# Kernel optimization log

Measured on AMD Instinct MI355X. Metric: run time of the kernel, lower is better.

The kernel has to match this reference:

```python
import jax, jax.numpy as jnp
import numpy as np

N_NODES = 20000
N_EDGES = 320000
T = 12
IN_DIM = 128
HID = 256
OUT = 128
HEADS = 4
NEG_SLOPE = 0.2


def _glorot(key, shape, fan_in):
    return jax.random.normal(key, shape, jnp.float32) * (1.0 / np.sqrt(fan_in))


def setup_inputs() -> dict:
    key = jax.random.key(0)
    ks = jax.random.split(key, 12)
    x = jax.random.normal(ks[0], (N_NODES, T, IN_DIM), jnp.float32)
    edge_index = jax.random.randint(ks[1], (2, N_EDGES), 0, N_NODES, jnp.int64)
    return {
        "x": x,
        "edge_index": edge_index,
        "W1": _glorot(ks[2], (IN_DIM, HID), IN_DIM),
        "a_src1": _glorot(ks[3], (HEADS, HID // HEADS), HID // HEADS),
        "a_dst1": _glorot(ks[4], (HEADS, HID // HEADS), HID // HEADS),
        "b1": jnp.zeros((HID,), jnp.float32),
        "W2": _glorot(ks[5], (HID, HID), HID),
        "a_src2": _glorot(ks[6], (HEADS, HID // HEADS), HID // HEADS),
        "a_dst2": _glorot(ks[7], (HEADS, HID // HEADS), HID // HEADS),
        "b2": jnp.zeros((HID,), jnp.float32),
        "W3": _glorot(ks[8], (HID, OUT), HID),
        "a_src3": _glorot(ks[9], (HEADS, OUT // HEADS), OUT // HEADS),
        "a_dst3": _glorot(ks[10], (HEADS, OUT // HEADS), OUT // HEADS),
        "b3": jnp.zeros((OUT,), jnp.float32),
    }


def gat_conv(x, src, dst, W, a_src, a_dst, bias):
    # GATConv (v1), concat=True, add_self_loops=False, negative_slope=0.2
    n = x.shape[0]
    H, C = a_src.shape
    h = (x @ W).reshape(n, H, C)                       # [N,H,C]
    alpha_s = jnp.sum(h * a_src[None], axis=-1)        # [N,H]
    alpha_d = jnp.sum(h * a_dst[None], axis=-1)        # [N,H]
    e = jax.nn.leaky_relu(alpha_s[src] + alpha_d[dst], NEG_SLOPE)  # [E,H]
    e_max = jax.ops.segment_max(e, dst, num_segments=n)           # [N,H]
    e_max = jnp.where(jnp.isfinite(e_max), e_max, 0.0)
    w = jnp.exp(e - e_max[dst])                        # [E,H]
    denom = jax.ops.segment_sum(w, dst, num_segments=n)           # [N,H]
    alpha = w / (denom[dst] + 1e-16)                   # [E,H]
    msg = h[src] * alpha[:, :, None]                   # [E,H,C]
    out = jax.ops.segment_sum(msg, dst, num_segments=n)           # [N,H,C]
    return out.reshape(n, H * C) + bias


def reference(x, edge_index, W1, a_src1, a_dst1, b1, W2, a_src2, a_dst2, b2,
              W3, a_src3, a_dst3, b3):
    src, dst = edge_index[0], edge_index[1]

    def net(xt):  # xt: [N, F]
        h = jax.nn.relu(gat_conv(xt, src, dst, W1, a_src1, a_dst1, b1))
        h = jax.nn.relu(gat_conv(h, src, dst, W2, a_src2, a_dst2, b2))
        return gat_conv(h, src, dst, W3, a_src3, a_dst3, b3)

    xt = jnp.transpose(x, (1, 0, 2))                   # [T,N,F]
    _, out = jax.lax.scan(lambda c, xi: (c, net(xi)), None, xt)
    return jnp.transpose(out, (1, 0, 2))               # [N,T,OUT]
```

## Files before the change

### kernel.cpp

```cpp
#include <hip/hip_runtime.h>
#include <cstdint>
#include <cstddef>
#include <type_traits>

#define N_NODES 20000
#define N_EDGES 320000
#define T_STEPS 12
#define HEADS   4
#define NEG_SLOPE 0.2f

typedef unsigned short u16;
typedef unsigned int   u32;

using bf16x8 = __attribute__((ext_vector_type(8))) __bf16;
using f32x4v = __attribute__((ext_vector_type(4))) float;


__global__ void hist_kernel(const int* __restrict__ dst, int* __restrict__ cnt) {
    int e = blockIdx.x * 256 + threadIdx.x;
    if (e < N_EDGES) atomicAdd(&cnt[dst[e]], 1);
}

__global__ __launch_bounds__(1024) void scan_kernel(const int* __restrict__ cnt,
                                                    int* __restrict__ rp) {
    __shared__ int sd[1024];
    __shared__ int sbase;
    int tid = threadIdx.x;
    if (tid == 0) sbase = 0;
    __syncthreads();
    for (int chunk = 0; chunk < N_NODES; chunk += 1024) {
        int i = chunk + tid;
        int v = (i < N_NODES) ? cnt[i] : 0;
        sd[tid] = v;
        __syncthreads();
        #pragma unroll
        for (int off = 1; off < 1024; off <<= 1) {
            int t = (tid >= off) ? sd[tid - off] : 0;
            __syncthreads();
            sd[tid] += t;
            __syncthreads();
        }
        int incl = sd[tid];
        int base = sbase;
        if (i < N_NODES) rp[i] = base + incl - v;
        __syncthreads();
        if (tid == 1023) sbase = base + incl;
        __syncthreads();
    }
    if (tid == 0) rp[N_NODES] = sbase;
}

__global__ void scatter_kernel(const int* __restrict__ src, const int* __restrict__ dst,
                               const int* __restrict__ rp, int* __restrict__ tmp,
                               int* __restrict__ col) {
    int e = blockIdx.x * 256 + threadIdx.x;
    if (e < N_EDGES) {
        int d = dst[e];
        int pos = rp[d] + atomicAdd(&tmp[d], 1);
        col[pos] = src[e];
    }
}


#define SPLIT2(fx, fy, H, L) do {                                          \
    u32 u0_ = __float_as_uint(fx), u1_ = __float_as_uint(fy);              \
    u32 r0_ = u0_ + 0x7fffu + ((u0_ >> 16) & 1u);                          \
    u32 r1_ = u1_ + 0x7fffu + ((u1_ >> 16) & 1u);                          \
    (H) = (r1_ & 0xffff0000u) | (r0_ >> 16);                               \
    float e0_ = (fx) - __uint_as_float(r0_ & 0xffff0000u);                 \
    float e1_ = (fy) - __uint_as_float(r1_ & 0xffff0000u);                 \
    u32 v0_ = __float_as_uint(e0_), v1_ = __float_as_uint(e1_);            \
    v0_ += 0x7fffu + ((v0_ >> 16) & 1u);                                   \
    v1_ += 0x7fffu + ((v1_ >> 16) & 1u);                                   \
    (L) = (v1_ & 0xffff0000u) | (v0_ >> 16);                               \
} while (0)

__global__ void wsplit_kernel(const float* __restrict__ W, u16* __restrict__ Wh,
                              u16* __restrict__ Wl, int K, int N) {
    int idx = blockIdx.x * 256 + threadIdx.x;
    if (idx >= K * N) return;
    int k = idx / N, n = idx - k * N;
    float f = W[idx];
    u32 u = __float_as_uint(f);
    u32 r = u + 0x7fffu + ((u >> 16) & 1u);
    u16 hb = (u16)(r >> 16);
    float lf = f - __uint_as_float(r & 0xffff0000u);
    u32 v = __float_as_uint(lf);
    v = v + 0x7fffu + ((v >> 16) & 1u);
    Wh[(size_t)n * K + k] = hb;
    Wl[(size_t)n * K + k] = (u16)(v >> 16);
}


template <typename AT>
__global__ __launch_bounds__(256) void gemm_mfma(
        const AT* __restrict__ A, const u16* __restrict__ Bh,
        const u16* __restrict__ Bl, _Float16* __restrict__ Y,
        int Mrows, int Ncols, int K, int strideT, int tbase, int nT) {
    constexpr bool A_F32 = std::is_same<AT, float>::value;
    __shared__ u16 As_h[128][40];
    __shared__ u16 As_l[128][40];
    __shared__ u16 Bs_h[128][40];
    __shared__ u16 Bs_l[128][40];

    int tid  = threadIdx.x;
    int wave = tid >> 6, lane = tid & 63;
    int wr = wave >> 1, wc = wave & 1;
    int fr = lane & 15, fg = lane >> 4;
    int row0 = blockIdx.x * 128;
    int col0 = blockIdx.y * 128;

    int am = tid >> 1;
    int ak = (tid & 1) << 4;
    const AT* ap = nullptr;
    {
        int r = row0 + am;
        if (r < Mrows) {
            int n = r / nT, tl = r - n * nT;
            ap = A + ((size_t)n * strideT + (size_t)(tbase + tl)) * (size_t)K + ak;
        }
    }
    int bn = tid >> 1;
    int bk = (tid & 1) << 4;
    const u16* bph = Bh + (size_t)(col0 + bn) * K + bk;
    const u16* bpl = Bl + (size_t)(col0 + bn) * K + bk;

    f32x4v acc[4][4] = {};

    float4 fa4[4];
    uint4  ra[2];
    uint4 vbh0, vbh1, vbl0, vbl1;

#define LOAD_TILE(K0) do {                                                  \
    if (ap) {                                                               \
        if (A_F32) {                                                        \
            const float* p_ = (const float*)ap + (K0);                      \
            fa4[0] = *(const float4*)(p_);      fa4[1] = *(const float4*)(p_ + 4);  \
            fa4[2] = *(const float4*)(p_ + 8);  fa4[3] = *(const float4*)(p_ + 12); \
        } else {                                                            \
            const _Float16* p_ = (const _Float16*)ap + (K0);                \
            ra[0] = *(const uint4*)(p_);  ra[1] = *(const uint4*)(p_ + 8);  \
        }                                                                   \
    } else {                                                                \
        fa4[0] = fa4[1] = fa4[2] = fa4[3] = make_float4(0.f, 0.f, 0.f, 0.f);\
        ra[0] = ra[1] = make_uint4(0, 0, 0, 0);                             \
    }                                                                       \
    vbh0 = *(const uint4*)(bph + (K0));  vbh1 = *(const uint4*)(bph + (K0) + 8); \
    vbl0 = *(const uint4*)(bpl + (K0));  vbl1 = *(const uint4*)(bpl + (K0) + 8); \
} while (0)

    LOAD_TILE(0);

    for (int k0 = 0; k0 < K; k0 += 32) {
        float fv[16];
        if (A_F32) {
            fv[0]=fa4[0].x; fv[1]=fa4[0].y; fv[2]=fa4[0].z; fv[3]=fa4[0].w;
            fv[4]=fa4[1].x; fv[5]=fa4[1].y; fv[6]=fa4[1].z; fv[7]=fa4[1].w;
            fv[8]=fa4[2].x; fv[9]=fa4[2].y; fv[10]=fa4[2].z; fv[11]=fa4[2].w;
            fv[12]=fa4[3].x; fv[13]=fa4[3].y; fv[14]=fa4[3].z; fv[15]=fa4[3].w;
        } else {
            const _Float16* hx = (const _Float16*)ra;
            #pragma unroll
            for (int i = 0; i < 16; ++i) fv[i] = (float)hx[i];
        }
        u32 h0, h1, h2, h3, h4, h5, h6, h7;
        u32 l0, l1, l2, l3, l4, l5, l6, l7;
        SPLIT2(fv[0],  fv[1],  h0, l0); SPLIT2(fv[2],  fv[3],  h1, l1);
        SPLIT2(fv[4],  fv[5],  h2, l2); SPLIT2(fv[6],  fv[7],  h3, l3);
        SPLIT2(fv[8],  fv[9],  h4, l4); SPLIT2(fv[10], fv[11], h5, l5);
        SPLIT2(fv[12], fv[13], h6, l6); SPLIT2(fv[14], fv[15], h7, l7);
        *(uint4*)&As_h[am][ak]     = make_uint4(h0, h1, h2, h3);
        *(uint4*)&As_h[am][ak + 8] = make_uint4(h4, h5, h6, h7);
        *(uint4*)&As_l[am][ak]     = make_uint4(l0, l1, l2, l3);
        *(uint4*)&As_l[am][ak + 8] = make_uint4(l4, l5, l6, l7);
        *(uint4*)&Bs_h[bn][bk]     = vbh0;
        *(uint4*)&Bs_h[bn][bk + 8] = vbh1;
        *(uint4*)&Bs_l[bn][bk]     = vbl0;
        *(uint4*)&Bs_l[bn][bk + 8] = vbl1;
        __syncthreads();

        if (k0 + 32 < K) LOAD_TILE(k0 + 32);

        bf16x8 fah[4], fal[4], fbh[4], fbl[4];
        #pragma unroll
        for (int i = 0; i < 4; ++i) {
            fah[i] = *(const bf16x8*)&As_h[wr * 64 + i * 16 + fr][fg * 8];
            fal[i] = *(const bf16x8*)&As_l[wr * 64 + i * 16 + fr][fg * 8];
        }
        #pragma unroll
        for (int j = 0; j < 4; ++j) {
            fbh[j] = *(const bf16x8*)&Bs_h[wc * 64 + j * 16 + fr][fg * 8];
            fbl[j] = *(const bf16x8*)&Bs_l[wc * 64 + j * 16 + fr][fg * 8];
        }
        #pragma unroll
        for (int i = 0; i < 4; ++i)
            #pragma unroll
            for (int j = 0; j < 4; ++j) {
                acc[i][j] = __builtin_amdgcn_mfma_f32_16x16x32_bf16(fah[i], fbh[j], acc[i][j], 0, 0, 0);
                acc[i][j] = __builtin_amdgcn_mfma_f32_16x16x32_bf16(fah[i], fbl[j], acc[i][j], 0, 0, 0);
                acc[i][j] = __builtin_amdgcn_mfma_f32_16x16x32_bf16(fal[i], fbh[j], acc[i][j], 0, 0, 0);
            }
        __syncthreads();
    }
#undef LOAD_TILE

    #pragma unroll
    for (int i = 0; i < 4; ++i) {
        #pragma unroll
        for (int q = 0; q < 4; ++q) {
            int rr = row0 + wr * 64 + i * 16 + fg * 4 + q;
            if (rr < Mrows) {
                _Float16* yp = Y + (size_t)rr * Ncols + col0 + wc * 64 + fr;
                #pragma unroll
                for (int j = 0; j < 4; ++j) yp[j * 16] = (_Float16)acc[i][j][q];
            }
        }
    }
}


template <int C>
__global__ __launch_bounds__(256) void alpha_kernel(
        const _Float16* __restrict__ h, const float* __restrict__ a_src,
        const float* __restrict__ a_dst, float* __restrict__ as,
        float* __restrict__ ad, int Mrows) {
    constexpr int HC = HEADS * C;
    constexpr int V  = HC / 64;
    int r = blockIdx.x * 4 + (threadIdx.x >> 6);
    if (r >= Mrows) return;
    int lane = threadIdx.x & 63;
    int ch0 = lane * V;
    int head = lane >> 4;
    const _Float16* hp = h + (size_t)r * HC + ch0;
    float s = 0.f, d = 0.f;
    #pragma unroll
    for (int i = 0; i < V; ++i) {
        float v = (float)hp[i];
        s = fmaf(v, a_src[ch0 + i], s);
        d = fmaf(v, a_dst[ch0 + i], d);
    }
    #pragma unroll
    for (int off = 1; off < 16; off <<= 1) {
        s += __shfl_xor(s, off);
        d += __shfl_xor(d, off);
    }
    if ((lane & 15) == 0) {
        as[(size_t)r * HEADS + head] = s;
        ad[(size_t)r * HEADS + head] = d;
    }
}


template <int NTOT, int NT, int C, bool RELU, bool TO_OUT, typename OutT>
__global__ __launch_bounds__(HEADS * C) void agg_kernel(
        const _Float16* __restrict__ h, const float* __restrict__ as,
        const float* __restrict__ ad, const int* __restrict__ rp,
        const int* __restrict__ col, const float* __restrict__ bias,
        OutT* __restrict__ out, int t0) {
    constexpr int HC  = HEADS * C;
    constexpr int NW  = HC / 64;
    constexpr int HPW = HEADS / NW;
    constexpr int CHUNK = 64;
    constexpr int WSTR = NT * HEADS + 1;
    constexpr int CG  = HC / 8;
    constexpr int EP  = HC / CG;

    __shared__ int   s_col[CHUNK];
    __shared__ float s_w[CHUNK][WSTR];
    __shared__ float s_red[NW][NT][HC];
    __shared__ float s_inv[NT][HEADS];

    int n = blockIdx.x;
    int tbase = blockIdx.y * NT;
    int tid = threadIdx.x;
    int wave = tid >> 6, lane = tid & 63;

    int beg = rp[n], end = rp[n + 1];

    float dsum[HPW][NT], adv[HPW][NT];
    #pragma unroll
    for (int hp = 0; hp < HPW; ++hp) {
        int head = wave + hp * NW;
        #pragma unroll
        for (int t = 0; t < NT; ++t) {
            dsum[hp][t] = 0.f;
            adv[hp][t] = ad[((size_t)n * NTOT + tbase + t) * HEADS + head];
        }
    }

    int cg = tid & (CG - 1);
    int eg = tid / CG;
    int hcg = (cg * 8) / C;
    float acc[NT][8];
    #pragma unroll
    for (int t = 0; t < NT; ++t)
        #pragma unroll
        for (int j = 0; j < 8; ++j) acc[t][j] = 0.f;

    for (int c0 = beg; c0 < end; c0 += CHUNK) {
        int cnt = min(CHUNK, end - c0);
        if (tid < cnt) s_col[tid] = col[c0 + tid];
        __syncthreads();
        if (lane < cnt) {
            int s = s_col[lane];
            #pragma unroll
            for (int hp = 0; hp < HPW; ++hp) {
                int head = wave + hp * NW;
                #pragma unroll
                for (int t = 0; t < NT; ++t) {
                    float v = as[((size_t)s * NTOT + tbase + t) * HEADS + head] + adv[hp][t];
                    v = v > 0.f ? v : NEG_SLOPE * v;
                    v = fminf(v, 80.f);
                    float w = __expf(v);
                    dsum[hp][t] += w;
                    s_w[lane][t * HEADS + head] = w;
                }
            }
        }
        __syncthreads();
        for (int e = eg; e < cnt; e += EP) {
            int s = s_col[e];
            const _Float16* hb = h + ((size_t)s * NTOT + tbase) * HC + cg * 8;
            #pragma unroll
            for (int t = 0; t < NT; ++t) {
                float w = s_w[e][t * HEADS + hcg];
                uint4 hv = *(const uint4*)(hb + (size_t)t * HC);
                const _Float16* hx = (const _Float16*)&hv;
                #pragma unroll
                for (int j = 0; j < 8; ++j)
                    acc[t][j] = fmaf((float)hx[j], w, acc[t][j]);
            }
        }
        __syncthreads();
    }

    #pragma unroll
    for (int off = 32; off; off >>= 1)
        #pragma unroll
        for (int hp = 0; hp < HPW; ++hp)
            #pragma unroll
            for (int t = 0; t < NT; ++t)
                dsum[hp][t] += __shfl_xor(dsum[hp][t], off);
    if (lane == 0) {
        #pragma unroll
        for (int hp = 0; hp < HPW; ++hp)
            #pragma unroll
            for (int t = 0; t < NT; ++t)
                s_inv[t][wave + hp * NW] = 1.f / (dsum[hp][t] + 1e-16f);
    }

    #pragma unroll
    for (int off = CG; off < 64; off <<= 1)
        #pragma unroll
        for (int t = 0; t < NT; ++t)
            #pragma unroll
            for (int j = 0; j < 8; ++j)
                acc[t][j] += __shfl_xor(acc[t][j], off);
    if (lane < CG) {
        #pragma unroll
        for (int t = 0; t < NT; ++t) {
            *(float4*)&s_red[wave][t][lane * 8] =
                make_float4(acc[t][0], acc[t][1], acc[t][2], acc[t][3]);
            *(float4*)&s_red[wave][t][lane * 8 + 4] =
                make_float4(acc[t][4], acc[t][5], acc[t][6], acc[t][7]);
        }
    }
    __syncthreads();

    int head_b = tid / C;
    float bv = bias[tid];
    #pragma unroll
    for (int t = 0; t < NT; ++t) {
        float o = 0.f;
        #pragma unroll
        for (int w = 0; w < NW; ++w) o += s_red[w][t][tid];
        o = o * s_inv[t][head_b] + bv;
        if (RELU) o = fmaxf(o, 0.f);
        if (TO_OUT)
            out[((size_t)n * T_STEPS + (size_t)(t0 + tbase + t)) * HC + tid] = (OutT)o;
        else
            out[((size_t)n * NTOT + tbase + t) * HC + tid] = (OutT)o;
    }
}


static inline size_t align256(size_t x) { return (x + 255) & ~(size_t)255; }

static size_t need_ws(int tc) {
    size_t s = 0;
    s += align256(sizeof(int) * (N_NODES + 1));
    s += align256(sizeof(int) * N_NODES);
    s += align256(sizeof(int) * N_EDGES);
    s += 2 * align256(2ull * 128 * 256);
    s += 2 * align256(2ull * 256 * 256);
    s += 2 * align256(2ull * 256 * 128);
    s += 2 * align256(4ull * tc * N_NODES * HEADS);
    s += align256(2ull * tc * N_NODES * 256);
    s += align256(2ull * tc * N_NODES * 256);
    return s;
}

struct Ptrs {
    const float *x, *W1, *av1, *aw1, *b1, *W2, *av2, *aw2, *b2, *W3, *av3, *aw3, *b3;
    float* out;
    int *rp, *col;
    u16 *w1h, *w1l, *w2h, *w2l, *w3h, *w3l;
    float *as_b, *ad_b;
    _Float16 *hbuf, *buf;
};

template <int NTOT>
static void run_chunk(const Ptrs& P, int t0, hipStream_t stream) {
    constexpr int NTA  = (NTOT % 3 == 0 && NTOT > 3) ? 3 : NTOT;
    constexpr int NSPL = NTOT / NTA;
    int Mrows = NTOT * N_NODES;
    dim3 gg1((Mrows + 127) / 128, 256 / 128);
    dim3 gg3((Mrows + 127) / 128, 128 / 128);
    dim3 ga(N_NODES, NSPL);
    int ablocks = (Mrows + 3) / 4;

    gemm_mfma<float><<<gg1, 256, 0, stream>>>(P.x, P.w1h, P.w1l, P.hbuf, Mrows, 256, 128, T_STEPS, t0, NTOT);
    alpha_kernel<64><<<ablocks, 256, 0, stream>>>(P.hbuf, P.av1, P.aw1, P.as_b, P.ad_b, Mrows);
    agg_kernel<NTOT, NTA, 64, true, false, _Float16><<<ga, 256, 0, stream>>>(
        P.hbuf, P.as_b, P.ad_b, P.rp, P.col, P.b1, P.buf, t0);

    gemm_mfma<_Float16><<<gg1, 256, 0, stream>>>(P.buf, P.w2h, P.w2l, P.hbuf, Mrows, 256, 256, NTOT, 0, NTOT);
    alpha_kernel<64><<<ablocks, 256, 0, stream>>>(P.hbuf, P.av2, P.aw2, P.as_b, P.ad_b, Mrows);
    agg_kernel<NTOT, NTA, 64, true, false, _Float16><<<ga, 256, 0, stream>>>(
        P.hbuf, P.as_b, P.ad_b, P.rp, P.col, P.b2, P.buf, t0);

    gemm_mfma<_Float16><<<gg3, 256, 0, stream>>>(P.buf, P.w3h, P.w3l, P.hbuf, Mrows, 128, 256, NTOT, 0, NTOT);
    alpha_kernel<32><<<ablocks, 256, 0, stream>>>(P.hbuf, P.av3, P.aw3, P.as_b, P.ad_b, Mrows);
    agg_kernel<NTOT, NTA, 32, false, true, float><<<ga, 128, 0, stream>>>(
        P.hbuf, P.as_b, P.ad_b, P.rp, P.col, P.b3, P.out, t0);
}

extern "C" void kernel_launch(void* const* d_in, const int* in_sizes, int n_in,
                              void* d_out, int out_size, void* d_ws, size_t ws_size,
                              hipStream_t stream) {
    Ptrs P;
    P.x   = (const float*)d_in[0];
    const int* eidx = (const int*)d_in[1];
    P.W1 = (const float*)d_in[2];  P.av1 = (const float*)d_in[3];
    P.aw1 = (const float*)d_in[4]; P.b1 = (const float*)d_in[5];
    P.W2 = (const float*)d_in[6];  P.av2 = (const float*)d_in[7];
    P.aw2 = (const float*)d_in[8]; P.b2 = (const float*)d_in[9];
    P.W3 = (const float*)d_in[10]; P.av3 = (const float*)d_in[11];
    P.aw3 = (const float*)d_in[12]; P.b3 = (const float*)d_in[13];
    P.out = (float*)d_out;

    const int* src = eidx;
    const int* dst = eidx + N_EDGES;

    int Tc = 1;
    const int cands[6] = {12, 6, 4, 3, 2, 1};
    for (int k = 0; k < 6; ++k) {
        if (need_ws(cands[k]) <= ws_size) { Tc = cands[k]; break; }
    }

    char* p = (char*)d_ws;
    P.rp  = (int*)p; p += align256(sizeof(int) * (N_NODES + 1));
    int* cnt = (int*)p; p += align256(sizeof(int) * N_NODES);
    P.col = (int*)p; p += align256(sizeof(int) * N_EDGES);
    P.w1h = (u16*)p; p += align256(2ull * 128 * 256);
    P.w1l = (u16*)p; p += align256(2ull * 128 * 256);
    P.w2h = (u16*)p; p += align256(2ull * 256 * 256);
    P.w2l = (u16*)p; p += align256(2ull * 256 * 256);
    P.w3h = (u16*)p; p += align256(2ull * 256 * 128);
    P.w3l = (u16*)p; p += align256(2ull * 256 * 128);
    P.as_b = (float*)p; p += align256(4ull * Tc * N_NODES * HEADS);
    P.ad_b = (float*)p; p += align256(4ull * Tc * N_NODES * HEADS);
    P.hbuf = (_Float16*)p; p += align256(2ull * Tc * N_NODES * 256);
    P.buf  = (_Float16*)p;

    hipMemsetAsync(cnt, 0, sizeof(int) * N_NODES, stream);
    hist_kernel<<<(N_EDGES + 255) / 256, 256, 0, stream>>>(dst, cnt);
    scan_kernel<<<1, 1024, 0, stream>>>(cnt, P.rp);
    hipMemsetAsync(cnt, 0, sizeof(int) * N_NODES, stream);
    scatter_kernel<<<(N_EDGES + 255) / 256, 256, 0, stream>>>(src, dst, P.rp, cnt, P.col);

    wsplit_kernel<<<(128 * 256 + 255) / 256, 256, 0, stream>>>(P.W1, P.w1h, P.w1l, 128, 256);
    wsplit_kernel<<<(256 * 256 + 255) / 256, 256, 0, stream>>>(P.W2, P.w2h, P.w2l, 256, 256);
    wsplit_kernel<<<(256 * 128 + 255) / 256, 256, 0, stream>>>(P.W3, P.w3h, P.w3l, 256, 128);

    for (int t0 = 0; t0 < T_STEPS; t0 += Tc) {
        switch (Tc) {
            case 12: run_chunk<12>(P, t0, stream); break;
            case 6:  run_chunk<6>(P, t0, stream); break;
            case 4:  run_chunk<4>(P, t0, stream); break;
            case 3:  run_chunk<3>(P, t0, stream); break;
            case 2:  run_chunk<2>(P, t0, stream); break;
            default: run_chunk<1>(P, t0, stream); break;
        }
    }
}
```

Before: 1.359 ms.

## Pre-split aggregation output into bf16 hi/lo and fuse attention logits into GEMM

The aggregation kernels for layers 1 and 2 now write their activations directly as bf16 high/low pairs. A new gemm_pair kernel consumes these pre-split operands, which removes the per-tile fp32/fp16-to-bf16 split inside the GEMM. That GEMM also computes the per-head source and destination attention dot products in its epilogue using shuffles, so the separate alpha_kernel launches for layers 2 and 3 are dropped. The cost is twice the activation buffer memory and twice the bytes written by aggregation and read by the GEMM.

Result: slower. 1.438 ms (+5.8%).

```diff
diff --git a/kernel.cpp b/kernel.cpp
--- a/kernel.cpp
+++ b/kernel.cpp
@@ -14,6 +14,12 @@
 
 using bf16x8 = __attribute__((ext_vector_type(8))) __bf16;
 using f32x4v = __attribute__((ext_vector_type(4))) float;
+
+__device__ __forceinline__ u16 bf16_rne(float f) {
+    u32 u = __float_as_uint(f);
+    u += 0x7fffu + ((u >> 16) & 1u);
+    return (u16)(u >> 16);
+}
 
 
 __global__ void hist_kernel(const int* __restrict__ dst, int* __restrict__ cnt) {
@@ -219,6 +225,142 @@
 }
 
 
+template <int CC>
+__global__ __launch_bounds__(256) void gemm_pair(
+        const u16* __restrict__ Ah, const u16* __restrict__ Al,
+        const u16* __restrict__ Bh, const u16* __restrict__ Bl,
+        _Float16* __restrict__ Y,
+        const float* __restrict__ a_src, const float* __restrict__ a_dst,
+        float* __restrict__ as_out, float* __restrict__ ad_out,
+        int Mrows, int Ncols, int K, int strideT, int tbase, int nT) {
+    __shared__ u16 As_h[128][40];
+    __shared__ u16 As_l[128][40];
+    __shared__ u16 Bs_h[128][40];
+    __shared__ u16 Bs_l[128][40];
+
+    int tid  = threadIdx.x;
+    int wave = tid >> 6, lane = tid & 63;
+    int wr = wave >> 1, wc = wave & 1;
+    int fr = lane & 15, fg = lane >> 4;
+    int row0 = blockIdx.x * 128;
+    int col0 = blockIdx.y * 128;
+
+    int am = tid >> 1;
+    int ak = (tid & 1) << 4;
+    size_t aoff = 0;
+    bool avalid = false;
+    {
+        int r = row0 + am;
+        if (r < Mrows) {
+            int n = r / nT, tl = r - n * nT;
+            aoff = ((size_t)n * strideT + (size_t)(tbase + tl)) * (size_t)K + ak;
+            avalid = true;
+        }
+    }
+    int bn = tid >> 1;
+    int bk = (tid & 1) << 4;
+    const u16* bph = Bh + (size_t)(col0 + bn) * K + bk;
+    const u16* bpl = Bl + (size_t)(col0 + bn) * K + bk;
+
+    f32x4v acc[4][4] = {};
+    uint4 rah0, rah1, ral0, ral1, rbh0, rbh1, rbl0, rbl1;
+
+#define LOAD_TILE(K0) do {                                                       \
+    if (avalid) {                                                                \
+        rah0 = *(const uint4*)(Ah + aoff + (K0));                                \
+        rah1 = *(const uint4*)(Ah + aoff + (K0) + 8);                            \
+        ral0 = *(const uint4*)(Al + aoff + (K0));                                \
+        ral1 = *(const uint4*)(Al + aoff + (K0) + 8);                            \
+    } else {                                                                     \
+        rah0 = rah1 = ral0 = ral1 = make_uint4(0, 0, 0, 0);                      \
+    }                                                                            \
+    rbh0 = *(const uint4*)(bph + (K0));  rbh1 = *(const uint4*)(bph + (K0) + 8); \
+    rbl0 = *(const uint4*)(bpl + (K0));  rbl1 = *(const uint4*)(bpl + (K0) + 8); \
+} while (0)
+
+    LOAD_TILE(0);
+
+    for (int k0 = 0; k0 < K; k0 += 32) {
+        *(uint4*)&As_h[am][ak]     = rah0;
+        *(uint4*)&As_h[am][ak + 8] = rah1;
+        *(uint4*)&As_l[am][ak]     = ral0;
+        *(uint4*)&As_l[am][ak + 8] = ral1;
+        *(uint4*)&Bs_h[bn][bk]     = rbh0;
+        *(uint4*)&Bs_h[bn][bk + 8] = rbh1;
+        *(uint4*)&Bs_l[bn][bk]     = rbl0;
+        *(uint4*)&Bs_l[bn][bk + 8] = rbl1;
+        __syncthreads();
+
+        if (k0 + 32 < K) LOAD_TILE(k0 + 32);
+
+        bf16x8 fah[4], fal[4], fbh[4], fbl[4];
+        #pragma unroll
+        for (int i = 0; i < 4; ++i) {
+            fah[i] = *(const bf16x8*)&As_h[wr * 64 + i * 16 + fr][fg * 8];
+            fal[i] = *(const bf16x8*)&As_l[wr * 64 + i * 16 + fr][fg * 8];
+        }
+        #pragma unroll
+        for (int j = 0; j < 4; ++j) {
+            fbh[j] = *(const bf16x8*)&Bs_h[wc * 64 + j * 16 + fr][fg * 8];
+            fbl[j] = *(const bf16x8*)&Bs_l[wc * 64 + j * 16 + fr][fg * 8];
+        }
+        #pragma unroll
+        for (int i = 0; i < 4; ++i)
+            #pragma unroll
+            for (int j = 0; j < 4; ++j) {
+                acc[i][j] = __builtin_amdgcn_mfma_f32_16x16x32_bf16(fah[i], fbh[j], acc[i][j], 0, 0, 0);
+                acc[i][j] = __builtin_amdgcn_mfma_f32_16x16x32_bf16(fah[i], fbl[j], acc[i][j], 0, 0, 0);
+                acc[i][j] = __builtin_amdgcn_mfma_f32_16x16x32_bf16(fal[i], fbh[j], acc[i][j], 0, 0, 0);
+            }
+        __syncthreads();
+    }
+#undef LOAD_TILE
+
+    constexpr int HPB = 64 / CC;
+    constexpr int JH  = 4 / HPB;
+    int headbase = (col0 + wc * 64) / CC;
+    float wvs[4], wvd[4];
+    #pragma unroll
+    for (int j = 0; j < 4; ++j) {
+        int c  = (j * 16 + fr) % CC;
+        int hd = headbase + j / JH;
+        wvs[j] = a_src[hd * CC + c];
+        wvd[j] = a_dst[hd * CC + c];
+    }
+    #pragma unroll
+    for (int i = 0; i < 4; ++i) {
+        #pragma unroll
+        for (int q = 0; q < 4; ++q) {
+            int rr = row0 + wr * 64 + i * 16 + fg * 4 + q;
+            if (rr < Mrows) {
+                _Float16* yp = Y + (size_t)rr * Ncols + col0 + wc * 64 + fr;
+                #pragma unroll
+                for (int j = 0; j < 4; ++j) yp[j * 16] = (_Float16)acc[i][j][q];
+                #pragma unroll
+                for (int hh = 0; hh < HPB; ++hh) {
+                    float sa = 0.f, sd = 0.f;
+                    #pragma unroll
+                    for (int jj = 0; jj < JH; ++jj) {
+                        int j = hh * JH + jj;
+                        sa = fmaf(acc[i][j][q], wvs[j], sa);
+                        sd = fmaf(acc[i][j][q], wvd[j], sd);
+                    }
+                    #pragma unroll
+                    for (int off = 1; off < 16; off <<= 1) {
+                        sa += __shfl_xor(sa, off);
+                        sd += __shfl_xor(sd, off);
+                    }
+                    if (fr == 0) {
+                        as_out[(size_t)rr * HEADS + headbase + hh] = sa;
+                        ad_out[(size_t)rr * HEADS + headbase + hh] = sd;
+                    }
+                }
+            }
+        }
+    }
+}
+
+
 template <int C>
 __global__ __launch_bounds__(256) void alpha_kernel(
         const _Float16* __restrict__ h, const float* __restrict__ a_src,
@@ -251,12 +393,13 @@
 }
 
 
-template <int NTOT, int NT, int C, bool RELU, bool TO_OUT, typename OutT>
+template <int NTOT, int NT, int C, bool RELU, bool TO_OUT, bool SPLIT>
 __global__ __launch_bounds__(HEADS * C) void agg_kernel(
         const _Float16* __restrict__ h, const float* __restrict__ as,
         const float* __restrict__ ad, const int* __restrict__ rp,
         const int* __restrict__ col, const float* __restrict__ bias,
-        OutT* __restrict__ out, int t0) {
+        float* __restrict__ out, u16* __restrict__ outh,
+        u16* __restrict__ outl, int t0) {
     constexpr int HC  = HEADS * C;
     constexpr int NW  = HC / 64;
     constexpr int HPW = HEADS / NW;
@@ -376,10 +519,15 @@
         for (int w = 0; w < NW; ++w) o += s_red[w][t][tid];
         o = o * s_inv[t][head_b] + bv;
         if (RELU) o = fmaxf(o, 0.f);
-        if (TO_OUT)
-            out[((size_t)n * T_STEPS + (size_t)(t0 + tbase + t)) * HC + tid] = (OutT)o;
-        else
-            out[((size_t)n * NTOT + tbase + t) * HC + tid] = (OutT)o;
+        if (TO_OUT) {
+            out[((size_t)n * T_STEPS + (size_t)(t0 + tbase + t)) * HC + tid] = o;
+        } else if (SPLIT) {
+            u16 hb16 = bf16_rne(o);
+            float lf = o - __uint_as_float(((u32)hb16) << 16);
+            size_t idx = ((size_t)n * NTOT + tbase + t) * HC + tid;
+            outh[idx] = hb16;
+            outl[idx] = bf16_rne(lf);
+        }
     }
 }
 
@@ -396,7 +544,7 @@
     s += 2 * align256(2ull * 256 * 128);
     s += 2 * align256(4ull * tc * N_NODES * HEADS);
     s += align256(2ull * tc * N_NODES * 256);
-    s += align256(2ull * tc * N_NODES * 256);
+    s += 2 * align256(2ull * tc * N_NODES * 256);
     return s;
 }
 
@@ -406,7 +554,8 @@
     int *rp, *col;
     u16 *w1h, *w1l, *w2h, *w2l, *w3h, *w3l;
     float *as_b, *ad_b;
-    _Float16 *hbuf, *buf;
+    _Float16 *hbuf;
+    u16 *bufh, *bufl;
 };
 
 template <int NTOT>
@@ -414,25 +563,27 @@
     constexpr int NTA  = (NTOT % 3 == 0 && NTOT > 3) ? 3 : NTOT;
     constexpr int NSPL = NTOT / NTA;
     int Mrows = NTOT * N_NODES;
-    dim3 gg1((Mrows + 127) / 128, 256 / 128);
-    dim3 gg3((Mrows + 127) / 128, 128 / 128);
+    dim3 gg1((Mrows + 127) / 128, 2);
+    dim3 gg3((Mrows + 127) / 128, 1);
     dim3 ga(N_NODES, NSPL);
     int ablocks = (Mrows + 3) / 4;
 
     gemm_mfma<float><<<gg1, 256, 0, stream>>>(P.x, P.w1h, P.w1l, P.hbuf, Mrows, 256, 128, T_STEPS, t0, NTOT);
     alpha_kernel<64><<<ablocks, 256, 0, stream>>>(P.hbuf, P.av1, P.aw1, P.as_b, P.ad_b, Mrows);
-    agg_kernel<NTOT, NTA, 64, true, false, _Float16><<<ga, 256, 0, stream>>>(
-        P.hbuf, P.as_b, P.ad_b, P.rp, P.col, P.b1, P.buf, t0);
-
-    gemm_mfma<_Float16><<<gg1, 256, 0, stream>>>(P.buf, P.w2h, P.w2l, P.hbuf, Mrows, 256, 256, NTOT, 0, NTOT);
-    alpha_kernel<64><<<ablocks, 256, 0, stream>>>(P.hbuf, P.av2, P.aw2, P.as_b, P.ad_b, Mrows);
-    agg_kernel<NTOT, NTA, 64, true, false, _Float16><<<ga, 256, 0, stream>>>(
-        P.hbuf, P.as_b, P.ad_b, P.rp, P.col, P.b2, P.buf, t0);
-
-    gemm_mfma<_Float16><<<gg3, 256, 0, stream>>>(P.buf, P.w3h, P.w3l, P.hbuf, Mrows, 128, 256, NTOT, 0, NTOT);
-    alpha_kernel<32><<<ablocks, 256, 0, stream>>>(P.hbuf, P.av3, P.aw3, P.as_b, P.ad_b, Mrows);
-    agg_kernel<NTOT, NTA, 32, false, true, float><<<ga, 128, 0, stream>>>(
-        P.hbuf, P.as_b, P.ad_b, P.rp, P.col, P.b3, P.out, t0);
+    agg_kernel<NTOT, NTA, 64, true, false, true><<<ga, 256, 0, stream>>>(
+        P.hbuf, P.as_b, P.ad_b, P.rp, P.col, P.b1, nullptr, P.bufh, P.bufl, t0);
+
+    gemm_pair<64><<<gg1, 256, 0, stream>>>(P.bufh, P.bufl, P.w2h, P.w2l, P.hbuf,
+                                           P.av2, P.aw2, P.as_b, P.ad_b,
+                                           Mrows, 256, 256, NTOT, 0, NTOT);
+    agg_kernel<NTOT, NTA, 64, true, false, true><<<ga, 256, 0, stream>>>(
+        P.hbuf, P.as_b, P.ad_b, P.rp, P.col, P.b2, nullptr, P.bufh, P.bufl, t0);
+
+    gemm_pair<32><<<gg3, 256, 0, stream>>>(P.bufh, P.bufl, P.w3h, P.w3l, P.hbuf,
+                                           P.av3, P.aw3, P.as_b, P.ad_b,
+                                           Mrows, 128, 256, NTOT, 0, NTOT);
+    agg_kernel<NTOT, NTA, 32, false, true, false><<<ga, 128, 0, stream>>>(
+        P.hbuf, P.as_b, P.ad_b, P.rp, P.col, P.b3, P.out, nullptr, nullptr, t0);
 }
 
 extern "C" void kernel_launch(void* const* d_in, const int* in_sizes, int n_in,
@@ -471,7 +622,8 @@
     P.as_b = (float*)p; p += align256(4ull * Tc * N_NODES * HEADS);
     P.ad_b = (float*)p; p += align256(4ull * Tc * N_NODES * HEADS);
     P.hbuf = (_Float16*)p; p += align256(2ull * Tc * N_NODES * 256);
-    P.buf  = (_Float16*)p;
+    P.bufh = (u16*)p; p += align256(2ull * Tc * N_NODES * 256);
+    P.bufl = (u16*)p;
 
     hipMemsetAsync(cnt, 0, sizeof(int) * N_NODES, stream);
     hist_kernel<<<(N_EDGES + 255) / 256, 256, 0, stream>>>(dst, cnt);
```
